# Kernel tuning notes

Measured on AMD Instinct MI355X. Metric: run time of the kernel, lower is better.

The kernel has to match this reference:

```python
import jax, jax.numpy as jnp
import numpy as np

WIN = 7
N = WIN * WIN            # 49 tokens per window
HEADS = 6
C = 192
NW = 4096                # windows per image
B_ = 8192                # batch * num_windows
EPS = 1e-12              # F.normalize eps


def _make_relative_position_index():
    # mirrors the torch buffer construction (torch.meshgrid default = 'ij')
    coords = np.stack(np.meshgrid(np.arange(WIN), np.arange(WIN), indexing='ij'))  # [2,7,7]
    flat = coords.reshape(2, -1)                                # [2,49]
    rel = flat[:, :, None] - flat[:, None, :]                   # [2,49,49]
    rel = rel.transpose(1, 2, 0).astype(np.int64)               # [49,49,2]
    rel[..., 0] += WIN - 1
    rel[..., 1] += WIN - 1
    rel[..., 0] *= 2 * WIN - 1
    return rel.sum(-1)                                          # [49,49], values in [0, 169)


def setup_inputs() -> dict:
    key = jax.random.key(0)
    ks = jax.random.split(key, 8)
    x = jax.random.normal(ks[0], (B_, N, C), dtype=jnp.float32)
    mask = jnp.zeros((NW, N, N), dtype=jnp.float32)
    d_l = jax.random.uniform(ks[1], (B_,), dtype=jnp.float32)
    w = 0.02
    Wq = jax.random.normal(ks[2], (C, C), dtype=jnp.float32) * w
    Wk = jax.random.normal(ks[3], (C, C), dtype=jnp.float32) * w
    Wv = jax.random.normal(ks[4], (C, C), dtype=jnp.float32) * w
    Wp = jax.random.normal(ks[5], (C, C), dtype=jnp.float32) * w
    temperature = jnp.ones((HEADS, 1, 1), dtype=jnp.float32)
    rpb_table = jax.random.normal(ks[6], ((2 * WIN - 1) ** 2, HEADS), dtype=jnp.float32) * w
    rel_index = jnp.asarray(_make_relative_position_index(), dtype=jnp.int32)
    return {"x": x, "mask": mask, "d_l": d_l, "Wq": Wq, "Wk": Wk, "Wv": Wv,
            "Wp": Wp, "temperature": temperature, "rpb_table": rpb_table,
            "rel_index": rel_index}


def _l2norm(t):
    # F.normalize(dim=-1): t / max(||t||_2, eps)
    n = jnp.sqrt(jnp.sum(t * t, axis=-1, keepdims=True))
    return t / jnp.maximum(n, EPS)


def reference(x, mask, d_l, Wq, Wk, Wv, Wp, temperature, rpb_table, rel_index):
    b, n, c = x.shape
    hd = c // HEADS  # head dim = 32

    def split_heads(t):
        return t.reshape(b, n, HEADS, hd).transpose(0, 2, 1, 3)  # b h n d

    q = split_heads(x @ Wq.T)
    k = split_heads(x @ Wk.T)
    v = split_heads(x @ Wv.T)

    q = _l2norm(q)
    k = _l2norm(k)

    attn = jnp.einsum('bhnd,bhmd->bhnm', q, k) * temperature  # temperature [h,1,1] broadcasts

    bias = rpb_table[rel_index.reshape(-1)].reshape(n, n, HEADS)  # gather [49,49,h]
    attn = attn + bias.transpose(2, 0, 1)[None]                   # [1,h,n,n]

    nW = mask.shape[0]
    attn = attn.reshape(b // nW, nW, HEADS, n, n) + mask[None, :, None]
    attn = attn.reshape(b, HEADS, n, n)

    attn = attn * d_l[:, None, None, None]  # degrade-level modulation
    attn = jax.nn.softmax(attn, axis=-1)

    out = jnp.einsum('bhnm,bhmd->bhnd', attn, v)
    out = out.transpose(0, 2, 1, 3).reshape(b, n, c)
    return out @ Wp.T
```

## Files before the change

### kernel.cpp

```cpp
#include <hip/hip_runtime.h>

#define NTOK 49
#define HEADS 6
#define CDIM 192
#define NWIN 4096

typedef unsigned short u16;
typedef unsigned int u32;
typedef unsigned long long u64;
typedef __attribute__((ext_vector_type(8))) __bf16 bf16x8;
typedef __attribute__((ext_vector_type(4))) float floatx4;

struct __attribute__((aligned(4))) F4 { float f[4]; };

#define OFF_X 0
#define OFF_Q 25600
#define OFF_K 51200
#define OFF_V 76800
#define OFF_P 104448
#define LDS_BYTES 141312

__device__ __forceinline__ u16 f2bf(float f) {
  return __builtin_bit_cast(u16, (__bf16)f);
}
__device__ __forceinline__ void st4bf(u16* p, float a, float b, float c, float d) {
  u32 lo = (u32)f2bf(a) | ((u32)f2bf(b) << 16);
  u32 hi = (u32)f2bf(c) | ((u32)f2bf(d) << 16);
  u64 t = (u64)lo | ((u64)hi << 32);
  *(u64*)p = t;
}
__device__ __forceinline__ float bf2f(u16 u) {
  union { u32 u; float f; } v; v.u = ((u32)u) << 16;
  return v.f;
}

__global__ __launch_bounds__(256)
void wprep(const float* __restrict__ Wq, const float* __restrict__ Wk,
           const float* __restrict__ Wv, const float* __restrict__ Wp,
           const float* __restrict__ rpb, const int* __restrict__ rel,
           u16* __restrict__ w_bf, float* __restrict__ bias) {
  const int tid = blockIdx.x * blockDim.x + threadIdx.x;
  const int stride = gridDim.x * blockDim.x;
  for (int i = tid; i < 4 * CDIM * CDIM; i += stride) {
    const int p = i / (CDIM * CDIM), e = i % (CDIM * CDIM);
    float v = (p == 0) ? Wq[e] : (p == 1) ? Wk[e] : (p == 2) ? Wv[e] : Wp[e];
    w_bf[i] = f2bf(v);
  }
  for (int i = tid; i < HEADS * NTOK * NTOK; i += stride) {
    const int h = i / (NTOK * NTOK), nm = i % (NTOK * NTOK);
    bias[i] = rpb[rel[nm] * HEADS + h];
  }
}

__global__ __launch_bounds__(1024)
void wattn_main(const float* __restrict__ x, const float* __restrict__ mask,
                const float* __restrict__ d_l, const float* __restrict__ temp,
                const u16* __restrict__ w_bf, const float* __restrict__ bias,
                float* __restrict__ out) {
  extern __shared__ __align__(16) char smem[];
  u16* Xb = (u16*)(smem + OFF_X);
  u16* Qn = (u16*)(smem + OFF_Q);
  u16* Kn = (u16*)(smem + OFF_K);
  u16* Vt = (u16*)(smem + OFF_V);
  u16* Pw = (u16*)(smem + OFF_P);

  const int b = blockIdx.x;
  const int tid = threadIdx.x;
  const int wave = tid >> 6;
  const int lane = tid & 63;
  const int g = lane >> 4;
  const int nl = lane & 15;

  {
    const float* xb = x + (size_t)b * (NTOK * CDIM);
    for (int i = tid; i < NTOK * 48; i += 1024) {
      const int n = i / 48;
      const int c = (i - n * 48) * 4;
      const float4 v = *(const float4*)(xb + n * CDIM + c);
      st4bf(Xb + n * 200 + c, v.x, v.y, v.z, v.w);
    }
    if (tid < 15 * 48) {
      const int n = NTOK + tid / 48;
      const int c = (tid % 48) * 4;
      *(u64*)(Xb + n * 200 + c) = 0ull;
    }
  }
  __syncthreads();

  for (int u = wave; u < 36; u += 16) {
    const int p = u / 12, o = u % 12;
    const u16* wb = w_bf + p * (CDIM * CDIM) + (o * 16 + nl) * CDIM + g * 8;
    floatx4 acc[4];
#pragma unroll
    for (int nt = 0; nt < 4; ++nt) acc[nt] = (floatx4){0.f, 0.f, 0.f, 0.f};
    if (p < 2) {
#pragma unroll
      for (int k = 0; k < 6; ++k) {
        const bf16x8 wf = *(const bf16x8*)(wb + k * 32);
#pragma unroll
        for (int nt = 0; nt < 4; ++nt) {
          const bf16x8 xk = *(const bf16x8*)(Xb + (nt * 16 + nl) * 200 + k * 32 + g * 8);
          acc[nt] = __builtin_amdgcn_mfma_f32_16x16x32_bf16(wf, xk, acc[nt], 0, 0, 0);
        }
      }
      u16* dst = (p == 0 ? Qn : Kn);
#pragma unroll
      for (int nt = 0; nt < 4; ++nt)
        st4bf(dst + (nt * 16 + nl) * 200 + o * 16 + g * 4,
              acc[nt][0], acc[nt][1], acc[nt][2], acc[nt][3]);
    } else {
#pragma unroll
      for (int k = 0; k < 6; ++k) {
        const bf16x8 wf = *(const bf16x8*)(wb + k * 32);
#pragma unroll
        for (int nt = 0; nt < 4; ++nt) {
          const bf16x8 xk = *(const bf16x8*)(Xb + (nt * 16 + nl) * 200 + k * 32 + g * 8);
          acc[nt] = __builtin_amdgcn_mfma_f32_16x16x32_bf16(xk, wf, acc[nt], 0, 0, 0);
        }
      }
#pragma unroll
      for (int nt = 0; nt < 4; ++nt)
        st4bf(Vt + (o * 16 + nl) * 72 + nt * 16 + g * 4,
              acc[nt][0], acc[nt][1], acc[nt][2], acc[nt][3]);
    }
  }
  __syncthreads();

  {
    const int sub = tid & 3;
    for (int ru = tid >> 2; ru < 2 * HEADS * NTOK; ru += 256) {
      const int t = ru / (HEADS * NTOK);
      const int rem = ru - t * (HEADS * NTOK);
      const int h = rem / NTOK, n = rem - h * NTOK;
      u16* base = (t == 0 ? Qn : Kn) + n * 200 + h * 32 + sub * 8;
      u64 lo = *(u64*)base;
      u64 hi = *(u64*)(base + 4);
      float f[8];
#pragma unroll
      for (int e = 0; e < 4; ++e) f[e] = bf2f((u16)(lo >> (16 * e)));
#pragma unroll
      for (int e = 0; e < 4; ++e) f[4 + e] = bf2f((u16)(hi >> (16 * e)));
      float ss = 0.f;
#pragma unroll
      for (int e = 0; e < 8; ++e) ss += f[e] * f[e];
      ss += __shfl_xor(ss, 1);
      ss += __shfl_xor(ss, 2);
      const float inv = 1.0f / fmaxf(sqrtf(ss), 1e-12f);
      st4bf(base, f[0] * inv, f[1] * inv, f[2] * inv, f[3] * inv);
      st4bf(base + 4, f[4] * inv, f[5] * inv, f[6] * inv, f[7] * inv);
    }
  }
  __syncthreads();

  {
    const float dl = d_l[b];
    const float LOG2E = 1.442695040888963f;
    const float dl2 = dl * LOG2E;
    const int wmask = b & (NWIN - 1);
    u16* Pb = Pw + wave * (16 * 72);
    for (int t = wave; t < 24; t += 16) {
      const int h = t >> 2, nt2 = t & 3;
      const int n = nt2 * 16 + nl;
      const int ncl = n < NTOK ? n : NTOK - 1;
      const float tdl = temp[h] * dl2;
      const bf16x8 qf = *(const bf16x8*)(Qn + n * 200 + h * 32 + g * 8);
      floatx4 sacc[4];
#pragma unroll
      for (int rt = 0; rt < 4; ++rt) {
        const bf16x8 kf = *(const bf16x8*)(Kn + (rt * 16 + nl) * 200 + h * 32 + g * 8);
        sacc[rt] = __builtin_amdgcn_mfma_f32_16x16x32_bf16(kf, qf, (floatx4){0.f, 0.f, 0.f, 0.f}, 0, 0, 0);
      }
      const float* brow = bias + (h * NTOK + ncl) * NTOK;
      const float* mrow = mask + ((size_t)wmask * NTOK + ncl) * NTOK;
      float L[4][4];
      float pmax = -1e30f;
#pragma unroll
      for (int rt = 0; rt < 3; ++rt) {
        const F4 b4 = *(const F4*)(brow + rt * 16 + g * 4);
        const F4 m4 = *(const F4*)(mrow + rt * 16 + g * 4);
#pragma unroll
        for (int r = 0; r < 4; ++r) {
          const float lv = fmaf(sacc[rt][r], tdl, (b4.f[r] + m4.f[r]) * dl2);
          L[rt][r] = lv;
          pmax = fmaxf(pmax, lv);
        }
      }
      {
        const float lv48 = fmaf(sacc[3][0], tdl, (brow[48] + mrow[48]) * dl2);
        L[3][0] = L[3][1] = L[3][2] = L[3][3] = -1e30f;
        if (g == 0) { L[3][0] = lv48; pmax = fmaxf(pmax, lv48); }
      }
      pmax = fmaxf(pmax, __shfl_xor(pmax, 16));
      pmax = fmaxf(pmax, __shfl_xor(pmax, 32));
      float psum = 0.f;
#pragma unroll
      for (int rt = 0; rt < 4; ++rt)
#pragma unroll
        for (int r = 0; r < 4; ++r) {
          const float e = exp2f(L[rt][r] - pmax);
          L[rt][r] = e;
          psum += e;
        }
      psum += __shfl_xor(psum, 16);
      psum += __shfl_xor(psum, 32);
      const float rinv = 1.0f / psum;
#pragma unroll
      for (int rt = 0; rt < 4; ++rt)
        st4bf(Pb + nl * 72 + rt * 16 + g * 4,
              L[rt][0] * rinv, L[rt][1] * rinv, L[rt][2] * rinv, L[rt][3] * rinv);
      floatx4 oacc[2];
      oacc[0] = (floatx4){0.f, 0.f, 0.f, 0.f};
      oacc[1] = (floatx4){0.f, 0.f, 0.f, 0.f};
#pragma unroll
      for (int ks = 0; ks < 2; ++ks) {
        const bf16x8 pf = *(const bf16x8*)(Pb + nl * 72 + ks * 32 + g * 8);
#pragma unroll
        for (int dt = 0; dt < 2; ++dt) {
          const bf16x8 vf = *(const bf16x8*)(Vt + (h * 32 + dt * 16 + nl) * 72 + ks * 32 + g * 8);
          oacc[dt] = __builtin_amdgcn_mfma_f32_16x16x32_bf16(vf, pf, oacc[dt], 0, 0, 0);
        }
      }
#pragma unroll
      for (int dt = 0; dt < 2; ++dt)
        st4bf(Xb + n * 200 + h * 32 + dt * 16 + g * 4,
              oacc[dt][0], oacc[dt][1], oacc[dt][2], oacc[dt][3]);
    }
  }
  __syncthreads();

  {
    float* outb = out + (size_t)b * (NTOK * CDIM);
    const u16* wpb = w_bf + 3 * (CDIM * CDIM);
    for (int o = wave; o < 12; o += 16) {
      const u16* wb = wpb + (o * 16 + nl) * CDIM + g * 8;
      floatx4 acc[4];
#pragma unroll
      for (int nt = 0; nt < 4; ++nt) acc[nt] = (floatx4){0.f, 0.f, 0.f, 0.f};
#pragma unroll
      for (int k = 0; k < 6; ++k) {
        const bf16x8 wf = *(const bf16x8*)(wb + k * 32);
#pragma unroll
        for (int nt = 0; nt < 4; ++nt) {
          const bf16x8 af = *(const bf16x8*)(Xb + (nt * 16 + nl) * 200 + k * 32 + g * 8);
          acc[nt] = __builtin_amdgcn_mfma_f32_16x16x32_bf16(wf, af, acc[nt], 0, 0, 0);
        }
      }
#pragma unroll
      for (int nt = 0; nt < 4; ++nt) {
        const int n = nt * 16 + nl;
        if (n < NTOK) {
          float4 v;
          v.x = acc[nt][0]; v.y = acc[nt][1]; v.z = acc[nt][2]; v.w = acc[nt][3];
          *(float4*)(outb + n * CDIM + o * 16 + g * 4) = v;
        }
      }
    }
  }
}

extern "C" void kernel_launch(void* const* d_in, const int* in_sizes, int n_in,
                              void* d_out, int out_size, void* d_ws, size_t ws_size,
                              hipStream_t stream) {
  const float* x    = (const float*)d_in[0];
  const float* mask = (const float*)d_in[1];
  const float* dl   = (const float*)d_in[2];
  const float* Wq   = (const float*)d_in[3];
  const float* Wk   = (const float*)d_in[4];
  const float* Wv   = (const float*)d_in[5];
  const float* Wp   = (const float*)d_in[6];
  const float* temp = (const float*)d_in[7];
  const float* rpb  = (const float*)d_in[8];
  const int*   rel  = (const int*)d_in[9];

  u16* w_bf = (u16*)d_ws;
  float* bias = (float*)((char*)d_ws + (size_t)4 * CDIM * CDIM * sizeof(u16));
  float* o = (float*)d_out;

  (void)hipFuncSetAttribute((const void*)wattn_main,
                            hipFuncAttributeMaxDynamicSharedMemorySize, LDS_BYTES);

  wprep<<<256, 256, 0, stream>>>(Wq, Wk, Wv, Wp, rpb, rel, w_bf, bias);
  wattn_main<<<8192, 1024, LDS_BYTES, stream>>>(x, mask, dl, temp, w_bf, bias, o);
}
```

Before: 581.0 us.

## Split GEMM work by token halves and fold L2 norm into scores

QKV and output projections now give each wave half the tokens. The wave keeps its X fragments in registers across all output tiles, so all 16 waves work instead of 9 (QKV) or 12 (projection). The separate Q/K normalization pass and its barrier are removed. Norms are computed per head in LDS and applied as row and column scales on the unnormalized QK^T scores. K fragments are also hoisted out of the row loop. This raises register pressure, and skipping the bf16 rounding of normalized Q/K changes numerics slightly.

```diff
diff --git a/kernel.cpp b/kernel.cpp
--- a/kernel.cpp
+++ b/kernel.cpp
@@ -10,6 +10,7 @@
 typedef unsigned long long u64;
 typedef __attribute__((ext_vector_type(8))) __bf16 bf16x8;
 typedef __attribute__((ext_vector_type(4))) float floatx4;
+typedef __attribute__((ext_vector_type(4))) u32 u32x4;
 
 struct __attribute__((aligned(4))) F4 { float f[4]; };
 
@@ -18,7 +19,8 @@
 #define OFF_K 51200
 #define OFF_V 76800
 #define OFF_P 104448
-#define LDS_BYTES 141312
+#define OFF_N 132096
+#define LDS_BYTES 138240
 
 __device__ __forceinline__ u16 f2bf(float f) {
   return __builtin_bit_cast(u16, (__bf16)f);
@@ -29,8 +31,12 @@
   u64 t = (u64)lo | ((u64)hi << 32);
   *(u64*)p = t;
 }
-__device__ __forceinline__ float bf2f(u16 u) {
-  union { u32 u; float f; } v; v.u = ((u32)u) << 16;
+__device__ __forceinline__ float bflo(u32 u) {
+  union { u32 u; float f; } v; v.u = u << 16;
+  return v.f;
+}
+__device__ __forceinline__ float bfhi(u32 u) {
+  union { u32 u; float f; } v; v.u = u & 0xffff0000u;
   return v.f;
 }
 
@@ -70,6 +76,7 @@
   const int lane = tid & 63;
   const int g = lane >> 4;
   const int nl = lane & 15;
+  const int half = wave & 1;
 
   {
     const float* xb = x + (size_t)b * (NTOK * CDIM);
@@ -87,89 +94,92 @@
   }
   __syncthreads();
 
-  for (int u = wave; u < 36; u += 16) {
-    const int p = u / 12, o = u % 12;
-    const u16* wb = w_bf + p * (CDIM * CDIM) + (o * 16 + nl) * CDIM + g * 8;
-    floatx4 acc[4];
-#pragma unroll
-    for (int nt = 0; nt < 4; ++nt) acc[nt] = (floatx4){0.f, 0.f, 0.f, 0.f};
-    if (p < 2) {
-#pragma unroll
-      for (int k = 0; k < 6; ++k) {
-        const bf16x8 wf = *(const bf16x8*)(wb + k * 32);
-#pragma unroll
-        for (int nt = 0; nt < 4; ++nt) {
-          const bf16x8 xk = *(const bf16x8*)(Xb + (nt * 16 + nl) * 200 + k * 32 + g * 8);
-          acc[nt] = __builtin_amdgcn_mfma_f32_16x16x32_bf16(wf, xk, acc[nt], 0, 0, 0);
-        }
-      }
-      u16* dst = (p == 0 ? Qn : Kn);
-#pragma unroll
-      for (int nt = 0; nt < 4; ++nt)
-        st4bf(dst + (nt * 16 + nl) * 200 + o * 16 + g * 4,
-              acc[nt][0], acc[nt][1], acc[nt][2], acc[nt][3]);
-    } else {
-#pragma unroll
-      for (int k = 0; k < 6; ++k) {
-        const bf16x8 wf = *(const bf16x8*)(wb + k * 32);
-#pragma unroll
-        for (int nt = 0; nt < 4; ++nt) {
-          const bf16x8 xk = *(const bf16x8*)(Xb + (nt * 16 + nl) * 200 + k * 32 + g * 8);
-          acc[nt] = __builtin_amdgcn_mfma_f32_16x16x32_bf16(xk, wf, acc[nt], 0, 0, 0);
-        }
-      }
-#pragma unroll
-      for (int nt = 0; nt < 4; ++nt)
-        st4bf(Vt + (o * 16 + nl) * 72 + nt * 16 + g * 4,
-              acc[nt][0], acc[nt][1], acc[nt][2], acc[nt][3]);
+  {
+    bf16x8 xf[2][6];
+#pragma unroll
+    for (int nt2 = 0; nt2 < 2; ++nt2)
+#pragma unroll
+      for (int k = 0; k < 6; ++k)
+        xf[nt2][k] = *(const bf16x8*)(Xb + (half * 32 + nt2 * 16 + nl) * 200 + k * 32 + g * 8);
+
+    for (int t = wave >> 1; t < 36; t += 8) {
+      const int p = t / 12, o = t - p * 12;
+      const u16* wb = w_bf + p * (CDIM * CDIM) + (o * 16 + nl) * CDIM + g * 8;
+      floatx4 acc[2];
+      acc[0] = (floatx4){0.f, 0.f, 0.f, 0.f};
+      acc[1] = (floatx4){0.f, 0.f, 0.f, 0.f};
+      if (p < 2) {
+#pragma unroll
+        for (int k = 0; k < 6; ++k) {
+          const bf16x8 wf = *(const bf16x8*)(wb + k * 32);
+          acc[0] = __builtin_amdgcn_mfma_f32_16x16x32_bf16(wf, xf[0][k], acc[0], 0, 0, 0);
+          acc[1] = __builtin_amdgcn_mfma_f32_16x16x32_bf16(wf, xf[1][k], acc[1], 0, 0, 0);
+        }
+        u16* dst = (p == 0 ? Qn : Kn);
+#pragma unroll
+        for (int nt2 = 0; nt2 < 2; ++nt2)
+          st4bf(dst + (half * 32 + nt2 * 16 + nl) * 200 + o * 16 + g * 4,
+                acc[nt2][0], acc[nt2][1], acc[nt2][2], acc[nt2][3]);
+      } else {
+#pragma unroll
+        for (int k = 0; k < 6; ++k) {
+          const bf16x8 wf = *(const bf16x8*)(wb + k * 32);
+          acc[0] = __builtin_amdgcn_mfma_f32_16x16x32_bf16(xf[0][k], wf, acc[0], 0, 0, 0);
+          acc[1] = __builtin_amdgcn_mfma_f32_16x16x32_bf16(xf[1][k], wf, acc[1], 0, 0, 0);
+        }
+#pragma unroll
+        for (int nt2 = 0; nt2 < 2; ++nt2)
+          st4bf(Vt + (o * 16 + nl) * 72 + half * 32 + nt2 * 16 + g * 4,
+                acc[nt2][0], acc[nt2][1], acc[nt2][2], acc[nt2][3]);
+      }
     }
   }
   __syncthreads();
 
-  {
-    const int sub = tid & 3;
-    for (int ru = tid >> 2; ru < 2 * HEADS * NTOK; ru += 256) {
-      const int t = ru / (HEADS * NTOK);
-      const int rem = ru - t * (HEADS * NTOK);
-      const int h = rem / NTOK, n = rem - h * NTOK;
-      u16* base = (t == 0 ? Qn : Kn) + n * 200 + h * 32 + sub * 8;
-      u64 lo = *(u64*)base;
-      u64 hi = *(u64*)(base + 4);
-      float f[8];
-#pragma unroll
-      for (int e = 0; e < 4; ++e) f[e] = bf2f((u16)(lo >> (16 * e)));
-#pragma unroll
-      for (int e = 0; e < 4; ++e) f[4 + e] = bf2f((u16)(hi >> (16 * e)));
-      float ss = 0.f;
-#pragma unroll
-      for (int e = 0; e < 8; ++e) ss += f[e] * f[e];
-      ss += __shfl_xor(ss, 1);
-      ss += __shfl_xor(ss, 2);
-      const float inv = 1.0f / fmaxf(sqrtf(ss), 1e-12f);
-      st4bf(base, f[0] * inv, f[1] * inv, f[2] * inv, f[3] * inv);
-      st4bf(base + 4, f[4] * inv, f[5] * inv, f[6] * inv, f[7] * inv);
-    }
-  }
-  __syncthreads();
-
-  {
+  if (wave < 12) {
+    const int h = wave >> 1;
+    float* nrmw = (float*)(smem + OFF_N) + wave * 128;
+    {
+      float ssk = 0.f, ssq = 0.f;
+      const u16* krow = Kn + lane * 200 + h * 32;
+      const u16* qrow = Qn + lane * 200 + h * 32;
+#pragma unroll
+      for (int j = 0; j < 4; ++j) {
+        const u32x4 kk = *(const u32x4*)(krow + j * 8);
+        const u32x4 qq = *(const u32x4*)(qrow + j * 8);
+#pragma unroll
+        for (int e = 0; e < 4; ++e) {
+          const float k0 = bflo(kk[e]), k1 = bfhi(kk[e]);
+          const float q0 = bflo(qq[e]), q1 = bfhi(qq[e]);
+          ssk = fmaf(k0, k0, fmaf(k1, k1, ssk));
+          ssq = fmaf(q0, q0, fmaf(q1, q1, ssq));
+        }
+      }
+      nrmw[lane] = 1.f / fmaxf(sqrtf(ssk), 1e-12f);
+      nrmw[64 + lane] = 1.f / fmaxf(sqrtf(ssq), 1e-12f);
+    }
     const float dl = d_l[b];
     const float LOG2E = 1.442695040888963f;
     const float dl2 = dl * LOG2E;
+    const float tdl = temp[h] * dl2;
     const int wmask = b & (NWIN - 1);
     u16* Pb = Pw + wave * (16 * 72);
-    for (int t = wave; t < 24; t += 16) {
-      const int h = t >> 2, nt2 = t & 3;
+    bf16x8 kf[4];
+#pragma unroll
+    for (int rt = 0; rt < 4; ++rt)
+      kf[rt] = *(const bf16x8*)(Kn + (rt * 16 + nl) * 200 + h * 32 + g * 8);
+
+#pragma unroll
+    for (int j = 0; j < 2; ++j) {
+      const int nt2 = (wave & 1) * 2 + j;
       const int n = nt2 * 16 + nl;
       const int ncl = n < NTOK ? n : NTOK - 1;
-      const float tdl = temp[h] * dl2;
       const bf16x8 qf = *(const bf16x8*)(Qn + n * 200 + h * 32 + g * 8);
       floatx4 sacc[4];
 #pragma unroll
-      for (int rt = 0; rt < 4; ++rt) {
-        const bf16x8 kf = *(const bf16x8*)(Kn + (rt * 16 + nl) * 200 + h * 32 + g * 8);
-        sacc[rt] = __builtin_amdgcn_mfma_f32_16x16x32_bf16(kf, qf, (floatx4){0.f, 0.f, 0.f, 0.f}, 0, 0, 0);
-      }
+      for (int rt = 0; rt < 4; ++rt)
+        sacc[rt] = __builtin_amdgcn_mfma_f32_16x16x32_bf16(kf[rt], qf, (floatx4){0.f, 0.f, 0.f, 0.f}, 0, 0, 0);
+      const float qr2 = nrmw[64 + n] * tdl;
       const float* brow = bias + (h * NTOK + ncl) * NTOK;
       const float* mrow = mask + ((size_t)wmask * NTOK + ncl) * NTOK;
       float L[4][4];
@@ -178,15 +188,16 @@
       for (int rt = 0; rt < 3; ++rt) {
         const F4 b4 = *(const F4*)(brow + rt * 16 + g * 4);
         const F4 m4 = *(const F4*)(mrow + rt * 16 + g * 4);
+        const F4 kr = *(const F4*)(nrmw + rt * 16 + g * 4);
 #pragma unroll
         for (int r = 0; r < 4; ++r) {
-          const float lv = fmaf(sacc[rt][r], tdl, (b4.f[r] + m4.f[r]) * dl2);
+          const float lv = fmaf(sacc[rt][r] * kr.f[r], qr2, (b4.f[r] + m4.f[r]) * dl2);
           L[rt][r] = lv;
           pmax = fmaxf(pmax, lv);
         }
       }
       {
-        const float lv48 = fmaf(sacc[3][0], tdl, (brow[48] + mrow[48]) * dl2);
+        const float lv48 = fmaf(sacc[3][0] * nrmw[48], qr2, (brow[48] + mrow[48]) * dl2);
         L[3][0] = L[3][1] = L[3][2] = L[3][3] = -1e30f;
         if (g == 0) { L[3][0] = lv48; pmax = fmaxf(pmax, lv48); }
       }
@@ -229,28 +240,32 @@
   __syncthreads();
 
   {
+    bf16x8 af[2][6];
+#pragma unroll
+    for (int nt2 = 0; nt2 < 2; ++nt2)
+#pragma unroll
+      for (int k = 0; k < 6; ++k)
+        af[nt2][k] = *(const bf16x8*)(Xb + (half * 32 + nt2 * 16 + nl) * 200 + k * 32 + g * 8);
     float* outb = out + (size_t)b * (NTOK * CDIM);
     const u16* wpb = w_bf + 3 * (CDIM * CDIM);
-    for (int o = wave; o < 12; o += 16) {
+    for (int s = wave; s < 24; s += 16) {
+      const int o = s >> 1;
       const u16* wb = wpb + (o * 16 + nl) * CDIM + g * 8;
-      floatx4 acc[4];
-#pragma unroll
-      for (int nt = 0; nt < 4; ++nt) acc[nt] = (floatx4){0.f, 0.f, 0.f, 0.f};
+      floatx4 acc[2];
+      acc[0] = (floatx4){0.f, 0.f, 0.f, 0.f};
+      acc[1] = (floatx4){0.f, 0.f, 0.f, 0.f};
 #pragma unroll
       for (int k = 0; k < 6; ++k) {
         const bf16x8 wf = *(const bf16x8*)(wb + k * 32);
-#pragma unroll
-        for (int nt = 0; nt < 4; ++nt) {
-          const bf16x8 af = *(const bf16x8*)(Xb + (nt * 16 + nl) * 200 + k * 32 + g * 8);
-          acc[nt] = __builtin_amdgcn_mfma_f32_16x16x32_bf16(wf, af, acc[nt], 0, 0, 0);
-        }
-      }
-#pragma unroll
-      for (int nt = 0; nt < 4; ++nt) {
-        const int n = nt * 16 + nl;
+        acc[0] = __builtin_amdgcn_mfma_f32_16x16x32_bf16(wf, af[0][k], acc[0], 0, 0, 0);
+        acc[1] = __builtin_amdgcn_mfma_f32_16x16x32_bf16(wf, af[1][k], acc[1], 0, 0, 0);
+      }
+#pragma unroll
+      for (int nt2 = 0; nt2 < 2; ++nt2) {
+        const int n = half * 32 + nt2 * 16 + nl;
         if (n < NTOK) {
           float4 v;
-          v.x = acc[nt][0]; v.y = acc[nt][1]; v.z = acc[nt][2]; v.w = acc[nt][3];
+          v.x = acc[nt2][0]; v.y = acc[nt2][1]; v.z = acc[nt2][2]; v.w = acc[nt2][3];
           *(float4*)(outb + n * CDIM + o * 16 + g * 4) = v;
         }
       }
```

New measurement: 769.7 us. 1.32x slower.

## Fold Q/K L2 normalization into attention score scaling, drop separate pass

Applied to the files above, without the earlier changes.

Removes the separate L2-normalization pass over Q and K in LDS, along with its block-wide barrier. Each wave now computes per-row inverse norms for its head into a small LDS scratch area and applies them as scale factors to the QK^T scores. Tasks are reassigned so each wave handles a single head, and the K fragments are loaded once per wave and reused across tasks. The cost is redundant norm computation per wave, extra LDS, and slightly different rounding because the raw, unnormalized bf16 Q/K feed the MFMA.

```diff
diff --git a/kernel.cpp b/kernel.cpp
--- a/kernel.cpp
+++ b/kernel.cpp
@@ -10,6 +10,7 @@
 typedef unsigned long long u64;
 typedef __attribute__((ext_vector_type(8))) __bf16 bf16x8;
 typedef __attribute__((ext_vector_type(4))) float floatx4;
+typedef __attribute__((ext_vector_type(4))) u32 u32x4;
 
 struct __attribute__((aligned(4))) F4 { float f[4]; };
 
@@ -18,7 +19,8 @@
 #define OFF_K 51200
 #define OFF_V 76800
 #define OFF_P 104448
-#define LDS_BYTES 141312
+#define OFF_N 141312
+#define LDS_BYTES 149504
 
 __device__ __forceinline__ u16 f2bf(float f) {
   return __builtin_bit_cast(u16, (__bf16)f);
@@ -29,8 +31,12 @@
   u64 t = (u64)lo | ((u64)hi << 32);
   *(u64*)p = t;
 }
-__device__ __forceinline__ float bf2f(u16 u) {
-  union { u32 u; float f; } v; v.u = ((u32)u) << 16;
+__device__ __forceinline__ float bflo(u32 u) {
+  union { u32 u; float f; } v; v.u = u << 16;
+  return v.f;
+}
+__device__ __forceinline__ float bfhi(u32 u) {
+  union { u32 u; float f; } v; v.u = u & 0xffff0000u;
   return v.f;
 }
 
@@ -127,49 +133,55 @@
   __syncthreads();
 
   {
-    const int sub = tid & 3;
-    for (int ru = tid >> 2; ru < 2 * HEADS * NTOK; ru += 256) {
-      const int t = ru / (HEADS * NTOK);
-      const int rem = ru - t * (HEADS * NTOK);
-      const int h = rem / NTOK, n = rem - h * NTOK;
-      u16* base = (t == 0 ? Qn : Kn) + n * 200 + h * 32 + sub * 8;
-      u64 lo = *(u64*)base;
-      u64 hi = *(u64*)(base + 4);
-      float f[8];
-#pragma unroll
-      for (int e = 0; e < 4; ++e) f[e] = bf2f((u16)(lo >> (16 * e)));
-#pragma unroll
-      for (int e = 0; e < 4; ++e) f[4 + e] = bf2f((u16)(hi >> (16 * e)));
-      float ss = 0.f;
-#pragma unroll
-      for (int e = 0; e < 8; ++e) ss += f[e] * f[e];
-      ss += __shfl_xor(ss, 1);
-      ss += __shfl_xor(ss, 2);
-      const float inv = 1.0f / fmaxf(sqrtf(ss), 1e-12f);
-      st4bf(base, f[0] * inv, f[1] * inv, f[2] * inv, f[3] * inv);
-      st4bf(base + 4, f[4] * inv, f[5] * inv, f[6] * inv, f[7] * inv);
-    }
-  }
-  __syncthreads();
-
-  {
     const float dl = d_l[b];
     const float LOG2E = 1.442695040888963f;
     const float dl2 = dl * LOG2E;
     const int wmask = b & (NWIN - 1);
     u16* Pb = Pw + wave * (16 * 72);
-    for (int t = wave; t < 24; t += 16) {
-      const int h = t >> 2, nt2 = t & 3;
+    float* nrmw = (float*)(smem + OFF_N) + wave * 128;
+
+    int t0, ntask;
+    if (wave < 8) { t0 = wave * 2; ntask = 2; }
+    else          { t0 = wave + 8; ntask = 1; }
+    const int h = t0 >> 2;
+
+    {
+      float ssk = 0.f, ssq = 0.f;
+      const u16* krow = Kn + lane * 200 + h * 32;
+      const u16* qrow = Qn + lane * 200 + h * 32;
+#pragma unroll
+      for (int j4 = 0; j4 < 4; ++j4) {
+        const u32x4 kk = *(const u32x4*)(krow + j4 * 8);
+        const u32x4 qq = *(const u32x4*)(qrow + j4 * 8);
+#pragma unroll
+        for (int e = 0; e < 4; ++e) {
+          const float k0 = bflo(kk[e]), k1 = bfhi(kk[e]);
+          const float q0 = bflo(qq[e]), q1 = bfhi(qq[e]);
+          ssk = fmaf(k0, k0, fmaf(k1, k1, ssk));
+          ssq = fmaf(q0, q0, fmaf(q1, q1, ssq));
+        }
+      }
+      nrmw[lane] = 1.f / fmaxf(sqrtf(ssk), 1e-12f);
+      nrmw[64 + lane] = 1.f / fmaxf(sqrtf(ssq), 1e-12f);
+    }
+
+    const float tdl = temp[h] * dl2;
+    bf16x8 kf[4];
+#pragma unroll
+    for (int rt = 0; rt < 4; ++rt)
+      kf[rt] = *(const bf16x8*)(Kn + (rt * 16 + nl) * 200 + h * 32 + g * 8);
+
+    for (int j = 0; j < ntask; ++j) {
+      const int t = t0 + j;
+      const int nt2 = t & 3;
       const int n = nt2 * 16 + nl;
       const int ncl = n < NTOK ? n : NTOK - 1;
-      const float tdl = temp[h] * dl2;
       const bf16x8 qf = *(const bf16x8*)(Qn + n * 200 + h * 32 + g * 8);
       floatx4 sacc[4];
 #pragma unroll
-      for (int rt = 0; rt < 4; ++rt) {
-        const bf16x8 kf = *(const bf16x8*)(Kn + (rt * 16 + nl) * 200 + h * 32 + g * 8);
-        sacc[rt] = __builtin_amdgcn_mfma_f32_16x16x32_bf16(kf, qf, (floatx4){0.f, 0.f, 0.f, 0.f}, 0, 0, 0);
-      }
+      for (int rt = 0; rt < 4; ++rt)
+        sacc[rt] = __builtin_amdgcn_mfma_f32_16x16x32_bf16(kf[rt], qf, (floatx4){0.f, 0.f, 0.f, 0.f}, 0, 0, 0);
+      const float qr2 = nrmw[64 + n] * tdl;
       const float* brow = bias + (h * NTOK + ncl) * NTOK;
       const float* mrow = mask + ((size_t)wmask * NTOK + ncl) * NTOK;
       float L[4][4];
@@ -178,15 +190,16 @@
       for (int rt = 0; rt < 3; ++rt) {
         const F4 b4 = *(const F4*)(brow + rt * 16 + g * 4);
         const F4 m4 = *(const F4*)(mrow + rt * 16 + g * 4);
+        const F4 kr = *(const F4*)(nrmw + rt * 16 + g * 4);
 #pragma unroll
         for (int r = 0; r < 4; ++r) {
-          const float lv = fmaf(sacc[rt][r], tdl, (b4.f[r] + m4.f[r]) * dl2);
+          const float lv = fmaf(sacc[rt][r] * kr.f[r], qr2, (b4.f[r] + m4.f[r]) * dl2);
           L[rt][r] = lv;
           pmax = fmaxf(pmax, lv);
         }
       }
       {
-        const float lv48 = fmaf(sacc[3][0], tdl, (brow[48] + mrow[48]) * dl2);
+        const float lv48 = fmaf(sacc[3][0] * nrmw[48], qr2, (brow[48] + mrow[48]) * dl2);
         L[3][0] = L[3][1] = L[3][2] = L[3][3] = -1e30f;
         if (g == 0) { L[3][0] = lv48; pmax = fmaxf(pmax, lv48); }
       }
```

Measured after the change: 549.4 us. -5.4%, faster.
